# Kernel optimization log

Measured on AMD Instinct MI355X. Metric: run time of the kernel, lower is better.

The kernel has to match this reference:

```python
import jax, jax.numpy as jnp
import numpy as np

N = 50000
E = 1600000
IN_C = 32
OUT_C = 32
OUT_SIZE = 1


def setup_inputs() -> dict:
    key = jax.random.key(0)
    ks = jax.random.split(key, 16)
    x = jax.random.normal(ks[0], (N, IN_C), dtype=jnp.float32)
    edge_index = jax.random.randint(ks[1], (2, E), 0, N, dtype=jnp.int64)

    def glorot(k, shape):
        lim = float(np.sqrt(6.0 / (shape[0] + shape[1])))
        return jax.random.uniform(k, shape, jnp.float32, -lim, lim)

    params = {
        # GCNConv weights for gates z, r, h: [in, out] and bias [out]
        'Wz_c': glorot(ks[2], (IN_C, OUT_C)), 'bz_c': jnp.zeros((OUT_C,), jnp.float32),
        'Wr_c': glorot(ks[3], (IN_C, OUT_C)), 'br_c': jnp.zeros((OUT_C,), jnp.float32),
        'Wh_c': glorot(ks[4], (IN_C, OUT_C)), 'bh_c': jnp.zeros((OUT_C,), jnp.float32),
        # GRU linear layers: [2*out, out] and bias [out]
        'Wz_l': glorot(ks[5], (2 * OUT_C, OUT_C)), 'bz_l': jnp.zeros((OUT_C,), jnp.float32),
        'Wr_l': glorot(ks[6], (2 * OUT_C, OUT_C)), 'br_l': jnp.zeros((OUT_C,), jnp.float32),
        'Wh_l': glorot(ks[7], (2 * OUT_C, OUT_C)), 'bh_l': jnp.zeros((OUT_C,), jnp.float32),
        # final readout Linear(out_channels, output_size)
        'W_lin': glorot(ks[8], (OUT_C, OUT_SIZE)), 'b_lin': jnp.zeros((OUT_SIZE,), jnp.float32),
    }
    return {'x': x, 'edge_index': edge_index, **params}


def _gcn_conv(x, W, b, src, dst, n_nodes):
    """GCNConv with add_self_loops=False, symmetric normalization."""
    h = x @ W  # [N, out]
    ones = jnp.ones((src.shape[0],), h.dtype)
    deg = jax.ops.segment_sum(ones, dst, num_segments=n_nodes)  # in-degree at targets
    dinv = jnp.where(deg > 0, jax.lax.rsqrt(jnp.maximum(deg, 1e-12)), 0.0)
    norm = dinv[src] * dinv[dst]  # [E]
    msg = h[src] * norm[:, None]  # gather + scale
    agg = jax.ops.segment_sum(msg, dst, num_segments=n_nodes)  # scatter-add
    return agg + b


def reference(x, edge_index, Wz_c, bz_c, Wr_c, br_c, Wh_c, bh_c,
              Wz_l, bz_l, Wr_l, br_l, Wh_l, bh_l, W_lin, b_lin):
    src, dst = edge_index[0], edge_index[1]
    n = x.shape[0]
    H = jnp.zeros((n, OUT_C), x.dtype)  # H=None -> zeros

    Z = jax.nn.sigmoid(jnp.concatenate([_gcn_conv(x, Wz_c, bz_c, src, dst, n), H], axis=1) @ Wz_l + bz_l)
    R = jax.nn.sigmoid(jnp.concatenate([_gcn_conv(x, Wr_c, br_c, src, dst, n), H], axis=1) @ Wr_l + br_l)
    H_tilde = jnp.tanh(jnp.concatenate([_gcn_conv(x, Wh_c, bh_c, src, dst, n), H * R], axis=1) @ Wh_l + bh_l)
    H = Z * H + (1.0 - Z) * H_tilde

    h = jax.nn.relu(H)
    return h @ W_lin + b_lin  # [N, output_size]
```

## Files before the change

### kernel.cpp

```cpp
#include <hip/hip_runtime.h>
#include <hip/hip_fp16.h>
#include <math.h>

#define NN 50000
#define NE 1600000
#define ELLW 80
#define SHN 6250
#define XH_WORDS 800000

#define NBIN 200
#define BINW 250
#define BINCAP 9000

#define OFF_ELL 0
#define NEED_A ((4000000ull + 800000 + 800000 + 50000 + 2112) * 4)
#define NEED_B ((4000000ull + 800000 + 50000 + 2112) * 4)

struct h2x2 { __half2 a, b; };

__global__ __launch_bounds__(1024) void init_kernel(
        const float* __restrict__ Wz_c, const float* __restrict__ bz_c,
        const float* __restrict__ Wh_c, const float* __restrict__ bh_c,
        const float* __restrict__ Wz_l, const float* __restrict__ bz_l,
        const float* __restrict__ Wh_l, const float* __restrict__ bh_l,
        float* __restrict__ Mz, float* __restrict__ Mh,
        float* __restrict__ cz, float* __restrict__ ch,
        unsigned int* __restrict__ bcur,
        const float* __restrict__ x, __half2* __restrict__ xh) {
    int t = threadIdx.x;
    if (blockIdx.x == 0) {
        int i = t >> 5, j = t & 31;
        float az = 0.0f, ah = 0.0f;
        for (int k = 0; k < 32; ++k) {
            az += Wz_c[i * 32 + k] * Wz_l[k * 32 + j];
            ah += Wh_c[i * 32 + k] * Wh_l[k * 32 + j];
        }
        Mz[i * 32 + j] = az;
        Mh[i * 32 + j] = ah;
        if (i == 0) {
            float sz = bz_l[j], sh = bh_l[j];
            for (int k = 0; k < 32; ++k) {
                sz += bz_c[k] * Wz_l[k * 32 + j];
                sh += bh_c[k] * Wh_l[k * 32 + j];
            }
            cz[j] = sz;
            ch[j] = sh;
        }
        return;
    }
    if (blockIdx.x == 1 && t < 256) bcur[t] = 0u;
    if (xh) {
        int idx = (blockIdx.x - 1) * 1024 + t;
        int stride = (gridDim.x - 1) * 1024;
        const float2* x2 = (const float2*)x;
        for (int i = idx; i < XH_WORDS; i += stride) {
            float2 v = x2[i];
            xh[i] = __floats2half2_rn(v.x, v.y);
        }
    }
}

__global__ __launch_bounds__(256) void bucket_kernel(const int* __restrict__ ei,
                                                     unsigned int* __restrict__ bcur,
                                                     unsigned int* __restrict__ bkt) {
    __shared__ unsigned int lcnt[NBIN];
    __shared__ unsigned int lstart[NBIN];
    __shared__ unsigned int loff[NBIN];
    __shared__ unsigned int gbase[NBIN];
    __shared__ unsigned int stage[8192];
    int t = threadIdx.x;
    for (int i = t; i < NBIN; i += 256) lcnt[i] = 0u;
    __syncthreads();
    int i4base = blockIdx.x * 2048;
    const int4* s4p = (const int4*)ei;
    const int4* d4p = (const int4*)(ei + NE);
    for (int ii = 0; ii < 8; ++ii) {
        int i4 = i4base + ii * 256 + t;
        if (i4 < NE / 4) {
            int4 s4 = s4p[i4];
            int4 d4 = d4p[i4];
#define CNT_E(dd, ss)                                                       \
            if ((unsigned)(dd) < NN && (unsigned)(ss) < NN)                 \
                atomicAdd(&lcnt[__umulhi((unsigned)(dd), 17179870u)], 1u);
            CNT_E(d4.x, s4.x) CNT_E(d4.y, s4.y) CNT_E(d4.z, s4.z) CNT_E(d4.w, s4.w)
#undef CNT_E
        }
    }
    __syncthreads();
    if (t < NBIN) loff[t] = lcnt[t];
    __syncthreads();
    for (int off = 1; off < NBIN; off <<= 1) {
        unsigned v = 0;
        if (t < NBIN && t >= off) v = loff[t - off];
        __syncthreads();
        if (t < NBIN) loff[t] += v;
        __syncthreads();
    }
    if (t < NBIN) {
        lstart[t] = loff[t] - lcnt[t];
        gbase[t] = lcnt[t] ? atomicAdd(&bcur[t], lcnt[t]) : 0u;
    }
    __syncthreads();
    if (t < NBIN) loff[t] = lstart[t];
    __syncthreads();
    for (int ii = 0; ii < 8; ++ii) {
        int i4 = i4base + ii * 256 + t;
        if (i4 < NE / 4) {
            int4 s4 = s4p[i4];
            int4 d4 = d4p[i4];
#define SC_E(dd, ss)                                                        \
            if ((unsigned)(dd) < NN && (unsigned)(ss) < NN) {               \
                unsigned bn = __umulhi((unsigned)(dd), 17179870u);          \
                unsigned p = atomicAdd(&loff[bn], 1u);                      \
                stage[p] = ((unsigned)(dd) << 16) | (unsigned)(ss);         \
            }
            SC_E(d4.x, s4.x) SC_E(d4.y, s4.y) SC_E(d4.z, s4.z) SC_E(d4.w, s4.w)
#undef SC_E
        }
    }
    __syncthreads();
    unsigned tot = loff[NBIN - 1];
    for (unsigned i = t; i < tot; i += 256) {
        unsigned v = stage[i];
        unsigned bn = __umulhi(v >> 16, 17179870u);
        unsigned g = gbase[bn] + (i - lstart[bn]);
        if (g < BINCAP) bkt[(size_t)bn * BINCAP + g] = v;
    }
}

__global__ __launch_bounds__(256) void build_ell_kernel(const unsigned int* __restrict__ bkt,
                                                        const unsigned int* __restrict__ bcur,
                                                        unsigned int* __restrict__ cnt,
                                                        float* __restrict__ dinv,
                                                        unsigned short* __restrict__ ell) {
    __shared__ unsigned int lcnt[BINW];
    __shared__ unsigned short stage[BINW * ELLW];
    int t = threadIdx.x;
    int b = blockIdx.x;
    int bin = (b & 7) * 25 + (b >> 3);
    int nbase = bin * BINW;
    for (int i = t; i < BINW; i += 256) lcnt[i] = 0u;
    __syncthreads();
    unsigned tot = bcur[bin]; if (tot > BINCAP) tot = BINCAP;
    const unsigned int* bp = bkt + (size_t)bin * BINCAP;
    for (unsigned i = t; i < tot; i += 256) {
        unsigned v = bp[i];
        unsigned ld = (v >> 16) - (unsigned)nbase;
        unsigned p = atomicAdd(&lcnt[ld], 1u);
        if (p < ELLW) stage[ld * ELLW + p] = (unsigned short)(v & 0xffffu);
    }
    __syncthreads();
    const unsigned int* st32 = (const unsigned int*)stage;
    unsigned int* ell32 = (unsigned int*)(ell + (size_t)nbase * ELLW);
    for (int i = t; i < BINW * ELLW / 2; i += 256) ell32[i] = st32[i];
    for (int i = t; i < BINW; i += 256) {
        unsigned d = lcnt[i];
        cnt[nbase + i] = d;
        dinv[nbase + i] = d ? rsqrtf((float)d) : 0.0f;
    }
}

template <int USE_H>
__global__ __launch_bounds__(256) void gather_node_kernel(const unsigned short* __restrict__ ell,
                                                          const unsigned int* __restrict__ cnt,
                                                          const float* __restrict__ dinv,
                                                          const float* __restrict__ x,
                                                          const h2x2* __restrict__ xh,
                                                          const float* __restrict__ Mz,
                                                          const float* __restrict__ Mh,
                                                          const float* __restrict__ cz,
                                                          const float* __restrict__ ch,
                                                          const float* __restrict__ Wlin,
                                                          const float* __restrict__ blin,
                                                          float* __restrict__ out) {
    __shared__ float sMz[1024], sMh[1024], scz[32], sch[32], sw[32];
    __shared__ float xs[4][32];
    int t = threadIdx.x;
    for (int i = t; i < 1024; i += 256) { sMz[i] = Mz[i]; sMh[i] = Mh[i]; }
    if (t < 32) { scz[t] = cz[t]; sch[t] = ch[t]; sw[t] = Wlin[t]; }
    __syncthreads();

    int w  = t >> 6;
    int l  = t & 63;
    int shard = blockIdx.x & 7;
    int grp   = blockIdx.x >> 3;
    int ns = grp * 4 + w;
    if (ns >= SHN) return;
    int n = shard * SHN + ns;

    int base = n * ELLW;
    int len  = (int)cnt[n];
    if (len > ELLW) len = ELLW;

    const float4* x4 = (const float4*)x;
    int es = l >> 3;
    int k  = l & 7;
    float4 acc = make_float4(0.f, 0.f, 0.f, 0.f);

    for (int c0 = 0; c0 < len; c0 += 64) {
        int m = len - c0; if (m > 64) m = 64;
        int s = 0; float wgt = 0.0f;
        if (l < m) { s = (int)ell[base + c0 + l]; wgt = dinv[s]; }
#define SW(j0) { int je = (j0) + es; int sj = __shfl(s, je); float wj = __shfl(wgt, je);   \
                 if (USE_H) {                                                              \
                     h2x2 hv = xh[sj * 8 + k];                                             \
                     float2 f0 = __half22float2(hv.a), f1 = __half22float2(hv.b);          \
                     acc.x += f0.x * wj; acc.y += f0.y * wj;                               \
                     acc.z += f1.x * wj; acc.w += f1.y * wj;                               \
                 } else {                                                                  \
                     float4 v = x4[sj * 8 + k];                                            \
                     acc.x += v.x * wj; acc.y += v.y * wj;                                 \
                     acc.z += v.z * wj; acc.w += v.w * wj;                                 \
                 } }
        SW(0) SW(8)
        if (m > 16) { SW(16) SW(24) }
        if (m > 32) { SW(32) SW(40) }
        if (m > 48) { SW(48) SW(56) }
#undef SW
    }
    #pragma unroll
    for (int mm = 8; mm < 64; mm <<= 1) {
        acc.x += __shfl_xor(acc.x, mm);
        acc.y += __shfl_xor(acc.y, mm);
        acc.z += __shfl_xor(acc.z, mm);
        acc.w += __shfl_xor(acc.w, mm);
    }
    if (es == 0) {
        float dn = dinv[n];
        float4* xs4 = (float4*)&xs[w][0];
        xs4[k] = make_float4(acc.x * dn, acc.y * dn, acc.z * dn, acc.w * dn);
    }

    int j = l & 31, half = l >> 5;
    float az = half ? 0.0f : scz[j];
    float ah = half ? 0.0f : sch[j];
    int ibase = half * 16;
    #pragma unroll
    for (int ii = 0; ii < 16; ++ii) {
        int i = ibase + ii;
        float v = xs[w][i];
        az += v * sMz[i * 32 + j];
        ah += v * sMh[i * 32 + j];
    }
    az += __shfl_xor(az, 32);
    ah += __shfl_xor(ah, 32);
    float z  = 1.0f / (1.0f + __expf(-az));
    float ht = tanhf(ah);
    float hv = (1.0f - z) * ht;
    hv = hv > 0.0f ? hv : 0.0f;
    float val = hv * sw[j];
    val += __shfl_xor(val, 1, 32);
    val += __shfl_xor(val, 2, 32);
    val += __shfl_xor(val, 4, 32);
    val += __shfl_xor(val, 8, 32);
    val += __shfl_xor(val, 16, 32);
    if (l == 0) out[n] = val + blin[0];
}

extern "C" void kernel_launch(void* const* d_in, const int* in_sizes, int n_in,
                              void* d_out, int out_size, void* d_ws, size_t ws_size,
                              hipStream_t stream) {
    const float* x    = (const float*)d_in[0];
    const int*   ei   = (const int*)d_in[1];
    const float* Wz_c = (const float*)d_in[2];
    const float* bz_c = (const float*)d_in[3];
    const float* Wh_c = (const float*)d_in[6];
    const float* bh_c = (const float*)d_in[7];
    const float* Wz_l = (const float*)d_in[8];
    const float* bz_l = (const float*)d_in[9];
    const float* Wh_l = (const float*)d_in[12];
    const float* bh_l = (const float*)d_in[13];
    const float* Wlin = (const float*)d_in[14];
    const float* blin = (const float*)d_in[15];
    float* out = (float*)d_out;
    float* ws = (float*)d_ws;

    int use_h = (ws_size >= NEED_A) ? 1 : 0;

    unsigned short* ell16 = (unsigned short*)(ws + OFF_ELL);
    unsigned int*   cnt   = (unsigned int*)(ws + 2000000);
    __half2*        xh    = use_h ? (__half2*)(ws + 2050000) : nullptr;
    float*          dinv  = ws + 2050000 + (use_h ? XH_WORDS : 0);
    float*          Mz    = dinv + NN;
    float*          Mh    = Mz + 1024;
    float*          cz    = Mh + 1024;
    float*          ch    = cz + 32;
    unsigned int*   bkt   = (unsigned int*)(ch + 32);
    unsigned int*   bcur  = bkt + (size_t)NBIN * BINCAP;

    const int bucket_grid = (NE / 4 + 2047) / 2048;
    const int build_grid  = NBIN;
    const int node_grid   = 8 * ((SHN + 3) / 4);
    const int init_grid   = 1 + 782;

    init_kernel<<<init_grid, 1024, 0, stream>>>(Wz_c, bz_c, Wh_c, bh_c,
                                                Wz_l, bz_l, Wh_l, bh_l,
                                                Mz, Mh, cz, ch, bcur, x, xh);
    bucket_kernel<<<bucket_grid, 256, 0, stream>>>(ei, bcur, bkt);
    build_ell_kernel<<<build_grid, 256, 0, stream>>>(bkt, bcur, cnt, dinv, ell16);
    if (use_h) {
        gather_node_kernel<1><<<node_grid, 256, 0, stream>>>(
            ell16, cnt, dinv, x, (const h2x2*)xh, Mz, Mh, cz, ch, Wlin, blin, out);
    } else {
        gather_node_kernel<0><<<node_grid, 256, 0, stream>>>(
            ell16, cnt, dinv, x, (const h2x2*)nullptr, Mz, Mh, cz, ch, Wlin, blin, out);
    }
}
```

Baseline: 160.1 us.

## Split edge buckets into sub-buckets and use finer bins with more blocks

Edge binning now uses 400 narrower bins, each split into 8 sub-buckets chosen by block index. This spreads the global atomic reservations and gives the ELL build more parallel blocks. The bucket kernel processes one int4 per thread with 512-thread blocks, so it launches many more, smaller blocks. The ELL copy widens to uint2, the gather kernel computes dinv from the count instead of loading it, and the fp16 convert grid shrinks. Risks: per-sub-bucket capacity overflow on skewed inputs, a larger workspace footprint, and count/scatter validity checks that no longer match for invalid sources.

```diff
diff --git a/kernel.cpp b/kernel.cpp
--- a/kernel.cpp
+++ b/kernel.cpp
@@ -8,9 +8,11 @@
 #define SHN 6250
 #define XH_WORDS 800000
 
-#define NBIN 200
-#define BINW 250
-#define BINCAP 9000
+#define NBIN 400
+#define BINW 125
+#define NSUB 8
+#define SUBCAP 680
+#define MAGIC125 34359739u
 
 #define OFF_ELL 0
 #define NEED_A ((4000000ull + 800000 + 800000 + 50000 + 2112) * 4)
@@ -48,7 +50,9 @@
         }
         return;
     }
-    if (blockIdx.x == 1 && t < 256) bcur[t] = 0u;
+    if (blockIdx.x == 1) {
+        for (int i = t; i < NBIN * NSUB; i += 1024) bcur[i] = 0u;
+    }
     if (xh) {
         int idx = (blockIdx.x - 1) * 1024 + t;
         int stride = (gridDim.x - 1) * 1024;
@@ -60,31 +64,28 @@
     }
 }
 
-__global__ __launch_bounds__(256) void bucket_kernel(const int* __restrict__ ei,
+__global__ __launch_bounds__(512) void bucket_kernel(const int* __restrict__ ei,
                                                      unsigned int* __restrict__ bcur,
                                                      unsigned int* __restrict__ bkt) {
     __shared__ unsigned int lcnt[NBIN];
     __shared__ unsigned int lstart[NBIN];
     __shared__ unsigned int loff[NBIN];
     __shared__ unsigned int gbase[NBIN];
-    __shared__ unsigned int stage[8192];
+    __shared__ unsigned int stage[2048];
     int t = threadIdx.x;
-    for (int i = t; i < NBIN; i += 256) lcnt[i] = 0u;
-    __syncthreads();
-    int i4base = blockIdx.x * 2048;
-    const int4* s4p = (const int4*)ei;
-    const int4* d4p = (const int4*)(ei + NE);
-    for (int ii = 0; ii < 8; ++ii) {
-        int i4 = i4base + ii * 256 + t;
-        if (i4 < NE / 4) {
-            int4 s4 = s4p[i4];
-            int4 d4 = d4p[i4];
-#define CNT_E(dd, ss)                                                       \
-            if ((unsigned)(dd) < NN && (unsigned)(ss) < NN)                 \
-                atomicAdd(&lcnt[__umulhi((unsigned)(dd), 17179870u)], 1u);
-            CNT_E(d4.x, s4.x) CNT_E(d4.y, s4.y) CNT_E(d4.z, s4.z) CNT_E(d4.w, s4.w)
+    for (int i = t; i < NBIN; i += 512) lcnt[i] = 0u;
+    __syncthreads();
+    int i4 = blockIdx.x * 512 + t;
+    bool valid = (i4 < NE / 4);
+    int4 s4 = make_int4(0, 0, 0, 0), d4 = make_int4(0, 0, 0, 0);
+    if (valid) {
+        s4 = ((const int4*)ei)[i4];
+        d4 = ((const int4*)(ei + NE))[i4];
+#define CNT_E(dd)                                                           \
+        if ((unsigned)(dd) < NN)                                            \
+            atomicAdd(&lcnt[__umulhi((unsigned)(dd), MAGIC125)], 1u);
+        CNT_E(d4.x) CNT_E(d4.y) CNT_E(d4.z) CNT_E(d4.w)
 #undef CNT_E
-        }
     }
     __syncthreads();
     if (t < NBIN) loff[t] = lcnt[t];
@@ -96,35 +97,31 @@
         if (t < NBIN) loff[t] += v;
         __syncthreads();
     }
+    int g = blockIdx.x & (NSUB - 1);
     if (t < NBIN) {
         lstart[t] = loff[t] - lcnt[t];
-        gbase[t] = lcnt[t] ? atomicAdd(&bcur[t], lcnt[t]) : 0u;
+        gbase[t] = lcnt[t] ? atomicAdd(&bcur[t * NSUB + g], lcnt[t]) : 0u;
     }
     __syncthreads();
     if (t < NBIN) loff[t] = lstart[t];
     __syncthreads();
-    for (int ii = 0; ii < 8; ++ii) {
-        int i4 = i4base + ii * 256 + t;
-        if (i4 < NE / 4) {
-            int4 s4 = s4p[i4];
-            int4 d4 = d4p[i4];
+    if (valid) {
 #define SC_E(dd, ss)                                                        \
-            if ((unsigned)(dd) < NN && (unsigned)(ss) < NN) {               \
-                unsigned bn = __umulhi((unsigned)(dd), 17179870u);          \
-                unsigned p = atomicAdd(&loff[bn], 1u);                      \
-                stage[p] = ((unsigned)(dd) << 16) | (unsigned)(ss);         \
-            }
-            SC_E(d4.x, s4.x) SC_E(d4.y, s4.y) SC_E(d4.z, s4.z) SC_E(d4.w, s4.w)
+        if ((unsigned)(dd) < NN && (unsigned)(ss) < NN) {                   \
+            unsigned bn = __umulhi((unsigned)(dd), MAGIC125);               \
+            unsigned p = atomicAdd(&loff[bn], 1u);                          \
+            stage[p] = ((unsigned)(dd) << 16) | (unsigned)(ss);             \
+        }
+        SC_E(d4.x, s4.x) SC_E(d4.y, s4.y) SC_E(d4.z, s4.z) SC_E(d4.w, s4.w)
 #undef SC_E
-        }
     }
     __syncthreads();
     unsigned tot = loff[NBIN - 1];
-    for (unsigned i = t; i < tot; i += 256) {
+    for (unsigned i = t; i < tot; i += 512) {
         unsigned v = stage[i];
-        unsigned bn = __umulhi(v >> 16, 17179870u);
-        unsigned g = gbase[bn] + (i - lstart[bn]);
-        if (g < BINCAP) bkt[(size_t)bn * BINCAP + g] = v;
+        unsigned bn = __umulhi(v >> 16, MAGIC125);
+        unsigned gg = gbase[bn] + (i - lstart[bn]);
+        if (gg < SUBCAP) bkt[(bn * NSUB + g) * SUBCAP + gg] = v;
     }
 }
 
@@ -134,25 +131,28 @@
                                                         float* __restrict__ dinv,
                                                         unsigned short* __restrict__ ell) {
     __shared__ unsigned int lcnt[BINW];
-    __shared__ unsigned short stage[BINW * ELLW];
+    __shared__ alignas(16) unsigned short stage[BINW * ELLW];
     int t = threadIdx.x;
     int b = blockIdx.x;
-    int bin = (b & 7) * 25 + (b >> 3);
+    int bin = (b & 7) * 50 + (b >> 3);
     int nbase = bin * BINW;
     for (int i = t; i < BINW; i += 256) lcnt[i] = 0u;
     __syncthreads();
-    unsigned tot = bcur[bin]; if (tot > BINCAP) tot = BINCAP;
-    const unsigned int* bp = bkt + (size_t)bin * BINCAP;
-    for (unsigned i = t; i < tot; i += 256) {
-        unsigned v = bp[i];
-        unsigned ld = (v >> 16) - (unsigned)nbase;
-        unsigned p = atomicAdd(&lcnt[ld], 1u);
-        if (p < ELLW) stage[ld * ELLW + p] = (unsigned short)(v & 0xffffu);
-    }
-    __syncthreads();
-    const unsigned int* st32 = (const unsigned int*)stage;
-    unsigned int* ell32 = (unsigned int*)(ell + (size_t)nbase * ELLW);
-    for (int i = t; i < BINW * ELLW / 2; i += 256) ell32[i] = st32[i];
+    for (int g = 0; g < NSUB; ++g) {
+        unsigned tot = bcur[bin * NSUB + g];
+        if (tot > SUBCAP) tot = SUBCAP;
+        const unsigned int* bp = bkt + (bin * NSUB + g) * SUBCAP;
+        for (unsigned i = t; i < tot; i += 256) {
+            unsigned v = bp[i];
+            unsigned ld = (v >> 16) - (unsigned)nbase;
+            unsigned p = atomicAdd(&lcnt[ld], 1u);
+            if (p < ELLW) stage[ld * ELLW + p] = (unsigned short)(v & 0xffffu);
+        }
+    }
+    __syncthreads();
+    const uint2* st2 = (const uint2*)stage;
+    uint2* ell2 = (uint2*)(ell + (size_t)nbase * ELLW);
+    for (int i = t; i < BINW * ELLW / 4; i += 256) ell2[i] = st2[i];
     for (int i = t; i < BINW; i += 256) {
         unsigned d = lcnt[i];
         cnt[nbase + i] = d;
@@ -189,8 +189,9 @@
     int n = shard * SHN + ns;
 
     int base = n * ELLW;
-    int len  = (int)cnt[n];
-    if (len > ELLW) len = ELLW;
+    int len0 = (int)cnt[n];
+    float dn = len0 ? rsqrtf((float)len0) : 0.0f;
+    int len = len0 > ELLW ? ELLW : len0;
 
     const float4* x4 = (const float4*)x;
     int es = l >> 3;
@@ -226,7 +227,6 @@
         acc.w += __shfl_xor(acc.w, mm);
     }
     if (es == 0) {
-        float dn = dinv[n];
         float4* xs4 = (float4*)&xs[w][0];
         xs4[k] = make_float4(acc.x * dn, acc.y * dn, acc.z * dn, acc.w * dn);
     }
@@ -286,17 +286,17 @@
     float*          cz    = Mh + 1024;
     float*          ch    = cz + 32;
     unsigned int*   bkt   = (unsigned int*)(ch + 32);
-    unsigned int*   bcur  = bkt + (size_t)NBIN * BINCAP;
-
-    const int bucket_grid = (NE / 4 + 2047) / 2048;
+    unsigned int*   bcur  = bkt + (size_t)NBIN * NSUB * SUBCAP;
+
+    const int bucket_grid = (NE / 4 + 511) / 512;
     const int build_grid  = NBIN;
     const int node_grid   = 8 * ((SHN + 3) / 4);
-    const int init_grid   = 1 + 782;
+    const int init_grid   = 1 + 256;
 
     init_kernel<<<init_grid, 1024, 0, stream>>>(Wz_c, bz_c, Wh_c, bh_c,
                                                 Wz_l, bz_l, Wh_l, bh_l,
                                                 Mz, Mh, cz, ch, bcur, x, xh);
-    bucket_kernel<<<bucket_grid, 256, 0, stream>>>(ei, bcur, bkt);
+    bucket_kernel<<<bucket_grid, 512, 0, stream>>>(ei, bcur, bkt);
     build_ell_kernel<<<build_grid, 256, 0, stream>>>(bkt, bcur, cnt, dinv, ell16);
     if (use_h) {
         gather_node_kernel<1><<<node_grid, 256, 0, stream>>>(
```

Result: no change. 160.1 us (+0.0%).
